# Performance work log

Measured on AMD Instinct MI355X. Metric: run time of the kernel, lower is better.

## Reference

```python
import jax, jax.numpy as jnp
import numpy as np

B, D, U, HU = 2048, 1024, 1024, 256

def _ln(x, eps=1e-3):
    # Keras LayerNormalization(center=False, scale=False), default epsilon=1e-3
    m = jnp.mean(x, axis=-1, keepdims=True)
    v = jnp.var(x, axis=-1, keepdims=True)
    return (x - m) * jax.lax.rsqrt(v + eps)

def setup_inputs() -> dict:
    key = jax.random.key(0)
    ks = jax.random.split(key, 17)
    s = 0.02
    return {
        "inputs": jax.random.normal(ks[0], (B, D), jnp.float32),
        "main_h": 0.1 * jax.random.normal(ks[1], (B, U), jnp.float32),
        "main_c": 0.1 * jax.random.normal(ks[2], (B, U), jnp.float32),
        "hyper_h": 0.1 * jax.random.normal(ks[3], (B, HU), jnp.float32),
        "hyper_c": 0.1 * jax.random.normal(ks[4], (B, HU), jnp.float32),
        "kernel": s * jax.random.normal(ks[5], (D, 4 * U), jnp.float32),
        "recurrent_kernel": s * jax.random.normal(ks[6], (U, 4 * U), jnp.float32),
        "bias": jnp.zeros((4 * U,), jnp.float32),
        "hyper_kernel": s * jax.random.normal(ks[7], (D + U, 4 * HU), jnp.float32),
        "hyper_rec_kernel": s * jax.random.normal(ks[8], (HU, 4 * HU), jnp.float32),
        "hyper_bias": jnp.zeros((4 * HU,), jnp.float32),
        "dx_w": s * jax.random.normal(ks[9], (HU, 4 * U), jnp.float32),
        "dx_b": s * jax.random.normal(ks[10], (4 * U,), jnp.float32),
        "dh_w": s * jax.random.normal(ks[11], (HU, 4 * U), jnp.float32),
        "dh_b": s * jax.random.normal(ks[12], (4 * U,), jnp.float32),
        "db_w": s * jax.random.normal(ks[13], (HU, 4 * U), jnp.float32),
        "db_b": s * jax.random.normal(ks[14], (4 * U,), jnp.float32),
    }

def reference(inputs, main_h, main_c, hyper_h, hyper_c,
              kernel, recurrent_kernel, bias,
              hyper_kernel, hyper_rec_kernel, hyper_bias,
              dx_w, dx_b, dh_w, dh_b, db_w, db_b):
    # --- hyper LSTMCell (Keras gate order i, f, g, o) ---
    hx = jnp.concatenate([inputs, main_h], axis=-1)          # [B, D+U]
    z = hx @ hyper_kernel + hyper_h @ hyper_rec_kernel + hyper_bias  # [B, 4*HU]
    hi, hf, hg, ho = jnp.split(z, 4, axis=-1)
    hyper_c_new = jax.nn.sigmoid(hf) * hyper_c + jax.nn.sigmoid(hi) * jnp.tanh(hg)
    hyper_out = jax.nn.sigmoid(ho) * jnp.tanh(hyper_c_new)  # = hyper_h_new

    # --- hypernet gate scalings ---
    d_x = hyper_out @ dx_w + dx_b                            # [B, 4*U]
    d_h = hyper_out @ dh_w + dh_b
    d_b = hyper_out @ db_w + db_b

    # --- main LSTM gates with hyper modulation + LayerNorm ---
    proj_x = inputs @ kernel + bias                          # [B, 4*U]
    proj_h = main_h @ recurrent_kernel                       # [B, 4*U]
    gates = _ln(d_x * proj_x + d_h * proj_h + d_b)
    i, f, g, o = jnp.split(gates, 4, axis=-1)
    main_c_new = jax.nn.sigmoid(f) * main_c + jax.nn.sigmoid(i) * jnp.tanh(g)
    main_h_new = jax.nn.sigmoid(o) * jnp.tanh(_ln(main_c_new))
    return (main_h_new, main_c_new, hyper_out, hyper_c_new)
```

## Files before the change

kernel.cpp:

```cpp
#include <hip/hip_runtime.h>
#include <cstdint>

typedef unsigned short u16;
typedef _Float16 half8 __attribute__((ext_vector_type(8)));
typedef float floatx4 __attribute__((ext_vector_type(4)));
typedef unsigned short ushort8v __attribute__((ext_vector_type(8)));
typedef float float4v __attribute__((ext_vector_type(4)));

#define BB 2048
#define UU 1024
#define HUx 256
#define O_H  0
#define O_C  (BB*UU)
#define O_HO (2*BB*UU)
#define O_HC (2*BB*UU + BB*HUx)
#define MFMAH __builtin_amdgcn_mfma_f32_16x16x32_f16

#define LBAR() do { \
    asm volatile("s_waitcnt lgkmcnt(0)\n\ts_barrier" ::: "memory"); \
    __builtin_amdgcn_sched_barrier(0); \
} while (0)

__device__ __forceinline__ float bf2f(u16 u) {
    union { uint32_t i; float f; } v; v.i = ((uint32_t)u) << 16; return v.f;
}
__device__ __forceinline__ u16 f2bf(float f) {
    union { float f; uint32_t i; } v; v.f = f;
    uint32_t r = v.i + 0x7fffu + ((v.i >> 16) & 1u);
    return (u16)(r >> 16);
}
__device__ __forceinline__ u16 f2h(float f) {
    _Float16 h = (_Float16)f; u16 u; __builtin_memcpy(&u, &h, 2); return u;
}
__device__ __forceinline__ float sigf(float x) { return 1.f / (1.f + expf(-x)); }
__device__ __forceinline__ float ldmix(const void* p, size_t i, int isbf) {
    return isbf ? bf2f(((const u16*)p)[i]) : ((const float*)p)[i];
}
__device__ __forceinline__ u16 ld2h(const void* p, size_t i, int isbf) {
    return f2h(ldmix(p, i, isbf));
}

__device__ __forceinline__ void ld128(half8 r[2], const u16* src, int row0, int ldK,
                                      int k0, int tid) {
    #pragma unroll
    for (int i = 0; i < 2; i++) {
        int v = tid + 256 * i;
        r[i] = *(const half8*)(src + (size_t)(row0 + (v >> 2)) * ldK + k0 + (v & 3) * 8);
    }
}
__device__ __forceinline__ void ld64(half8& r, const u16* src, int row0, int ldK,
                                     int k0, int tid) {
    r = *(const half8*)(src + (size_t)(row0 + (tid >> 2)) * ldK + k0 + (tid & 3) * 8);
}
__device__ __forceinline__ void wr128(u16* lds, const half8 r[2], int tid) {
    #pragma unroll
    for (int i = 0; i < 2; i++) {
        int v = tid + 256 * i;
        *(half8*)&lds[(v >> 2) * 40 + (v & 3) * 8] = r[i];
    }
}
__device__ __forceinline__ void wr64(u16* lds, half8 r, int tid) {
    *(half8*)&lds[(tid >> 2) * 40 + (tid & 3) * 8] = r;
}
__device__ __forceinline__ void wrS128(u16* lds, const half8 r[2], int tid) {
    #pragma unroll
    for (int i = 0; i < 2; i++) {
        int v = tid + 256 * i;
        int ps = (v & 3) ^ ((v >> 3) & 3);
        *(half8*)&lds[(v >> 2) * 32 + ps * 8] = r[i];
    }
}
__device__ __forceinline__ void wrS64(u16* lds, half8 r, int tid) {
    int ps = (tid & 3) ^ ((tid >> 3) & 3);
    *(half8*)&lds[(tid >> 2) * 32 + ps * 8] = r;
}

__device__ __forceinline__ int detect_local(const u16* raw) {
    int lane = threadIdx.x & 63;
    u16 u = raw[2 * lane];
    int e = (u >> 7) & 0xFF;
    unsigned long long m = __ballot(e >= 100 && e <= 134);
    return (__popcll(m) >= 32) ? 1 : 0;
}

__device__ __forceinline__ void transpose_tile(const void* in, u16* out, int C,
                                               int ostride, int ocol, int r0, int c0,
                                               int isbf, u16 th[32][33]) {
    int tid = threadIdx.x;
    int tx = tid & 31, ty = tid >> 5;
    #pragma unroll
    for (int i = 0; i < 32; i += 8)
        th[ty + i][tx] = ld2h(in, (size_t)(r0 + ty + i) * C + c0 + tx, isbf);
    __syncthreads();
    #pragma unroll
    for (int i = 0; i < 32; i += 8)
        out[(size_t)(c0 + ty + i) * ostride + ocol + r0 + tx] = th[tx][ty + i];
}

__global__ __launch_bounds__(256) void prep_all(
    const void* __restrict__ xs, const void* __restrict__ ms, const void* __restrict__ hs,
    const void* __restrict__ hyper_k, const void* __restrict__ hyper_rk,
    const void* __restrict__ kernel_w, const void* __restrict__ rec_w,
    const void* __restrict__ dx_w, const void* __restrict__ dh_w, const void* __restrict__ db_w,
    u16* __restrict__ xh, u16* __restrict__ mh, u16* __restrict__ hh,
    u16* __restrict__ BTh, u16* __restrict__ kT, u16* __restrict__ rkT,
    u16* __restrict__ dxT, u16* __restrict__ dhT, u16* __restrict__ dbT,
    int* __restrict__ flag) {
    __shared__ u16 th[32][33];
    int bid = blockIdx.x, tid = threadIdx.x;
    int isbf = detect_local((const u16*)xs);
    if (bid == 0 && tid == 0) *flag = isbf;

    if (bid < 2304) {
        int i = bid * 256 + tid;
        const void* src; u16* dst; int t;
        if (i < 262144)      { src = xs; dst = xh; t = i; }
        else if (i < 524288) { src = ms; dst = mh; t = i - 262144; }
        else                 { src = hs; dst = hh; t = i - 524288; }
        half8 o;
        if (isbf) {
            ushort8v v = *(const ushort8v*)((const u16*)src + (size_t)t * 8);
            #pragma unroll
            for (int j = 0; j < 8; j++) o[j] = (_Float16)bf2f(v[j]);
        } else {
            float4v a = *(const float4v*)((const float*)src + (size_t)t * 8);
            float4v b = *(const float4v*)((const float*)src + (size_t)t * 8 + 4);
            #pragma unroll
            for (int j = 0; j < 4; j++) { o[j] = (_Float16)a[j]; o[j + 4] = (_Float16)b[j]; }
        }
        *(half8*)(dst + (size_t)t * 8) = o;
    } else if (bid < 4352) {
        int u = bid - 2304;
        transpose_tile(hyper_k, BTh, 1024, 2304, 0, (u >> 5) * 32, (u & 31) * 32, isbf, th);
    } else if (bid < 4608) {
        int u = bid - 4352;
        transpose_tile(hyper_rk, BTh, 1024, 2304, 2048, (u >> 5) * 32, (u & 31) * 32, isbf, th);
    } else if (bid < 12800) {
        int u = bid - 4608;
        int z = u >> 12;
        int r = u & 4095;
        const void* in = z ? rec_w : kernel_w;
        u16* out = z ? rkT : kT;
        transpose_tile(in, out, 4096, 1024, 0, (r >> 7) * 32, (r & 127) * 32, isbf, th);
    } else {
        int u = bid - 12800;
        int z = u >> 10;
        int r = u & 1023;
        const void* in = (z == 0) ? dx_w : (z == 1) ? dh_w : db_w;
        u16* out = (z == 0) ? dxT : (z == 1) ? dhT : dbT;
        transpose_tile(in, out, 4096, 256, 0, (r >> 7) * 32, (r & 127) * 32, isbf, th);
    }
}

__device__ __forceinline__ void gh_load(half8 pA[2], half8& pB,
                                        const u16* xh, const u16* mh, const u16* hh,
                                        const u16* BT, int bm, int bn, int s, int tid) {
    const u16* Ap; int ldA, kA;
    if (s < 32)      { Ap = xh; ldA = 1024; kA = s * 32; }
    else if (s < 64) { Ap = mh; ldA = 1024; kA = (s - 32) * 32; }
    else             { Ap = hh; ldA = 256;  kA = (s - 64) * 32; }
    ld128(pA, Ap, bm, ldA, kA, tid);
    ld64(pB, BT, bn, 2304, s * 32, tid);
}

__global__ __launch_bounds__(256) void gemm_hyper(const u16* __restrict__ xh,
                                                  const u16* __restrict__ mh,
                                                  const u16* __restrict__ hh,
                                                  const u16* __restrict__ BT,
                                                  float* __restrict__ z) {
    __shared__ __align__(16) u16 sA[128 * 40];
    __shared__ __align__(16) u16 sB[64 * 40];
    int tid = threadIdx.x, lane = tid & 63, wave = tid >> 6;
    int wm = (wave & 1) * 64, wn = (wave >> 1) * 32;
    int bm = blockIdx.y * 128, bn = blockIdx.x * 64;
    int s0 = blockIdx.z * 36, s1 = s0 + 36;
    floatx4 acc[4][2] = {};
    int mr = lane & 15, kq = (lane >> 4) * 8;

    half8 pA[2]; half8 pB;
    gh_load(pA, pB, xh, mh, hh, BT, bm, bn, s0, tid);
    wr128(sA, pA, tid); wr64(sB, pB, tid);
    gh_load(pA, pB, xh, mh, hh, BT, bm, bn, s0 + 1, tid);
    LBAR();

    #pragma unroll 1
    for (int s = s0; s < s1; s++) {
        half8 a[4], b[2];
        #pragma unroll
        for (int t = 0; t < 4; t++) a[t] = *(const half8*)&sA[(wm + t * 16 + mr) * 40 + kq];
        #pragma unroll
        for (int t = 0; t < 2; t++) b[t] = *(const half8*)&sB[(wn + t * 16 + mr) * 40 + kq];
        #pragma unroll
        for (int tm = 0; tm < 4; tm++)
            #pragma unroll
            for (int tn = 0; tn < 2; tn++)
                acc[tm][tn] = MFMAH(a[tm], b[tn], acc[tm][tn], 0, 0, 0);
        LBAR();
        if (s < s1 - 1) {
            wr128(sA, pA, tid); wr64(sB, pB, tid);
            if (s < s1 - 2)
                gh_load(pA, pB, xh, mh, hh, BT, bm, bn, s + 2, tid);
            LBAR();
        }
    }

    float* zp = z + (size_t)blockIdx.z * 2048 * 1024;
    #pragma unroll
    for (int tm = 0; tm < 4; tm++)
        #pragma unroll
        for (int tn = 0; tn < 2; tn++) {
            int col = bn + wn + tn * 16 + (lane & 15);
            #pragma unroll
            for (int rr = 0; rr < 4; rr++) {
                int row = bm + wm + tm * 16 + (lane >> 4) * 4 + rr;
                zp[(size_t)row * 1024 + col] = acc[tm][tn][rr];
            }
        }
}

__global__ void hyper_cell(const float* __restrict__ z, const void* __restrict__ hyper_c,
                           const void* __restrict__ hyper_bias, void* __restrict__ out,
                           u16* __restrict__ ho16, const int* __restrict__ flag) {
    int isbf = *flag;
    int t = blockIdx.x * 256 + threadIdx.x;
    int k = t & 255;
    const float* zr  = z + (size_t)(t >> 8) * 1024;
    const float* zr2 = zr + (size_t)2048 * 1024;
    float hi = zr[k]       + zr2[k]       + ldmix(hyper_bias, k, isbf);
    float hf = zr[k + 256] + zr2[k + 256] + ldmix(hyper_bias, k + 256, isbf);
    float hg = zr[k + 512] + zr2[k + 512] + ldmix(hyper_bias, k + 512, isbf);
    float ho = zr[k + 768] + zr2[k + 768] + ldmix(hyper_bias, k + 768, isbf);
    float c  = ldmix(hyper_c, t, isbf);
    float cn = sigf(hf) * c + sigf(hi) * tanhf(hg);
    float hout = sigf(ho) * tanhf(cn);
    ho16[t] = f2h(hout);
    if (isbf) {
        ((u16*)out)[O_HO + t] = f2bf(hout);
        ((u16*)out)[O_HC + t] = f2bf(cn);
    } else {
        ((float*)out)[O_HO + t] = hout;
        ((float*)out)[O_HC + t] = cn;
    }
}

__global__ __launch_bounds__(256, 2) void mega_fused(
    const u16* __restrict__ xh, const u16* __restrict__ mh, const u16* __restrict__ ho16,
    const u16* __restrict__ kT, const u16* __restrict__ rkT,
    const u16* __restrict__ dxT, const u16* __restrict__ dhT, const u16* __restrict__ dbT,
    const void* __restrict__ bias, const void* __restrict__ dx_b,
    const void* __restrict__ dh_b, const void* __restrict__ db_b,
    u16* __restrict__ gp, const int* __restrict__ flag) {
    __shared__ __align__(16) u16 S[2][12288];
    int isbf = *flag;
    int tid = threadIdx.x, lane = tid & 63, wave = tid >> 6;
    int wm = (wave & 1) * 64, wn = (wave >> 1) * 32;
    int bm = blockIdx.y * 128, bn = blockIdx.x * 64;
    floatx4 apx[4][2] = {}, aph[4][2] = {}, adx[4][2] = {}, adh[4][2] = {}, adb[4][2] = {};
    int mr = lane & 15;
    int kqs = (((lane >> 4) ^ ((mr >> 1) & 3))) * 8;

    half8 nA1[2], nA2[2], nB1, nB2, nB3;

    ld128(nA1, xh,  bm, 1024, 0, tid);
    ld128(nA2, mh,  bm, 1024, 0, tid);
    ld64(nB1, kT,  bn, 1024, 0, tid);
    ld64(nB2, rkT, bn, 1024, 0, tid);
    wrS128(S[0], nA1, tid); wrS128(S[0] + 4096, nA2, tid);
    wrS64(S[0] + 8192, nB1, tid); wrS64(S[0] + 10240, nB2, tid);
    ld128(nA1, xh,  bm, 1024, 32, tid);
    ld128(nA2, mh,  bm, 1024, 32, tid);
    ld64(nB1, kT,  bn, 1024, 32, tid);
    ld64(nB2, rkT, bn, 1024, 32, tid);
    LBAR();

    #pragma unroll 1
    for (int k0 = 0; k0 < 1024; k0 += 32) {
        int p = (k0 >> 5) & 1;
        const u16* C = S[p];
        u16* N = S[p ^ 1];
        half8 ax[4], am[4], bk[2], br[2];
        #pragma unroll
        for (int t = 0; t < 4; t++) {
            int ra = (wm + t * 16 + mr) * 32 + kqs;
            ax[t] = *(const half8*)&C[ra];
            am[t] = *(const half8*)&C[4096 + ra];
        }
        #pragma unroll
        for (int t = 0; t < 2; t++) {
            int rb = (wn + t * 16 + mr) * 32 + kqs;
            bk[t] = *(const half8*)&C[8192 + rb];
            br[t] = *(const half8*)&C[10240 + rb];
        }
        if (k0 < 992) {
            wrS128(N, nA1, tid); wrS128(N + 4096, nA2, tid);
            wrS64(N + 8192, nB1, tid); wrS64(N + 10240, nB2, tid);
        } else {
            wrS128(N, nA1, tid);
            wrS64(N + 8192, nB1, tid); wrS64(N + 10240, nB2, tid); wrS64(N + 4096, nB3, tid);
        }
        if (k0 < 960) {
            ld128(nA1, xh,  bm, 1024, k0 + 64, tid);
            ld128(nA2, mh,  bm, 1024, k0 + 64, tid);
            ld64(nB1, kT,  bn, 1024, k0 + 64, tid);
            ld64(nB2, rkT, bn, 1024, k0 + 64, tid);
        } else if (k0 == 960) {
            ld128(nA1, ho16, bm, 256, 0, tid);
            ld64(nB1, dxT, bn, 256, 0, tid);
            ld64(nB2, dhT, bn, 256, 0, tid);
            ld64(nB3, dbT, bn, 256, 0, tid);
        } else {
            ld128(nA1, ho16, bm, 256, 32, tid);
            ld64(nB1, dxT, bn, 256, 32, tid);
            ld64(nB2, dhT, bn, 256, 32, tid);
            ld64(nB3, dbT, bn, 256, 32, tid);
        }
        #pragma unroll
        for (int tm = 0; tm < 4; tm++)
            #pragma unroll
            for (int tn = 0; tn < 2; tn++) {
                apx[tm][tn] = MFMAH(ax[tm], bk[tn], apx[tm][tn], 0, 0, 0);
                aph[tm][tn] = MFMAH(am[tm], br[tn], aph[tm][tn], 0, 0, 0);
            }
        LBAR();
    }

    #pragma unroll 1
    for (int k0 = 0; k0 < 256; k0 += 32) {
        int p = (k0 >> 5) & 1;
        const u16* C = S[p];
        u16* N = S[p ^ 1];
        half8 a[4], bx[2], bh[2], bb[2];
        #pragma unroll
        for (int t = 0; t < 4; t++) {
            int ra = (wm + t * 16 + mr) * 32 + kqs;
            a[t] = *(const half8*)&C[ra];
        }
        #pragma unroll
        for (int t = 0; t < 2; t++) {
            int rb = (wn + t * 16 + mr) * 32 + kqs;
            bx[t] = *(const half8*)&C[8192 + rb];
            bh[t] = *(const half8*)&C[10240 + rb];
            bb[t] = *(const half8*)&C[4096 + rb];
        }
        if (k0 < 224) {
            wrS128(N, nA1, tid);
            wrS64(N + 8192, nB1, tid); wrS64(N + 10240, nB2, tid); wrS64(N + 4096, nB3, tid);
        }
        if (k0 < 192) {
            ld128(nA1, ho16, bm, 256, k0 + 64, tid);
            ld64(nB1, dxT, bn, 256, k0 + 64, tid);
            ld64(nB2, dhT, bn, 256, k0 + 64, tid);
            ld64(nB3, dbT, bn, 256, k0 + 64, tid);
        }
        #pragma unroll
        for (int tm = 0; tm < 4; tm++)
            #pragma unroll
            for (int tn = 0; tn < 2; tn++) {
                adx[tm][tn] = MFMAH(a[tm], bx[tn], adx[tm][tn], 0, 0, 0);
                adh[tm][tn] = MFMAH(a[tm], bh[tn], adh[tm][tn], 0, 0, 0);
                adb[tm][tn] = MFMAH(a[tm], bb[tn], adb[tm][tn], 0, 0, 0);
            }
        LBAR();
    }

    #pragma unroll
    for (int tn = 0; tn < 2; tn++) {
        int col = bn + wn + tn * 16 + (lane & 15);
        float bv  = ldmix(bias, col, isbf);
        float dxb = ldmix(dx_b, col, isbf);
        float dhb = ldmix(dh_b, col, isbf);
        float dbb = ldmix(db_b, col, isbf);
        #pragma unroll
        for (int tm = 0; tm < 4; tm++) {
            #pragma unroll
            for (int rr = 0; rr < 4; rr++) {
                int row = bm + wm + tm * 16 + (lane >> 4) * 4 + rr;
                float px = apx[tm][tn][rr] + bv;
                float ph = aph[tm][tn][rr];
                float dx = adx[tm][tn][rr] + dxb;
                float dh = adh[tm][tn][rr] + dhb;
                float db = adb[tm][tn][rr] + dbb;
                gp[(size_t)row * 4096 + col] = f2h(dx * px + dh * ph + db);
            }
        }
    }
}

__device__ __forceinline__ void block_reduce2(float& a, float& b, float* red) {
    #pragma unroll
    for (int o = 32; o > 0; o >>= 1) {
        a += __shfl_down(a, o, 64);
        b += __shfl_down(b, o, 64);
    }
    int lane = threadIdx.x & 63, w = threadIdx.x >> 6;
    if (lane == 0) { red[w] = a; red[4 + w] = b; }
    __syncthreads();
    a = red[0] + red[1] + red[2] + red[3];
    b = red[4] + red[5] + red[6] + red[7];
    __syncthreads();
}

__global__ __launch_bounds__(256) void ln_main(const u16* __restrict__ gp,
                                               const void* __restrict__ main_c,
                                               void* __restrict__ out,
                                               const int* __restrict__ flag) {
    __shared__ float sPre[4096];
    __shared__ float sC[1024];
    __shared__ float red[8];
    int isbf = *flag;
    int b = blockIdx.x, tid = threadIdx.x;
    const u16* g = gp + (size_t)b * 4096;
    float s = 0.f, q = 0.f;
    for (int j0 = tid * 8; j0 < 4096; j0 += 2048) {
        half8 v = *(const half8*)(g + j0);
        #pragma unroll
        for (int e = 0; e < 8; e++) {
            float f = (float)v[e];
            sPre[j0 + e] = f; s += f; q += f * f;
        }
    }
    block_reduce2(s, q, red);
    float mean = s * (1.f / 4096.f);
    float var = q * (1.f / 4096.f) - mean * mean;
    float rs = rsqrtf(var + 1e-3f);
    float s2 = 0.f, q2 = 0.f;
    for (int u = tid; u < 1024; u += 256) {
        float gi = (sPre[u] - mean) * rs;
        float gf = (sPre[u + 1024] - mean) * rs;
        float gg = (sPre[u + 2048] - mean) * rs;
        float c = ldmix(main_c, (size_t)b * 1024 + u, isbf);
        float cn = sigf(gf) * c + sigf(gi) * tanhf(gg);
        sC[u] = cn;
        if (isbf) ((u16*)out)[O_C + (size_t)b * 1024 + u] = f2bf(cn);
        else      ((float*)out)[O_C + (size_t)b * 1024 + u] = cn;
        s2 += cn; q2 += cn * cn;
    }
    block_reduce2(s2, q2, red);
    float m2 = s2 * (1.f / 1024.f);
    float v2 = q2 * (1.f / 1024.f) - m2 * m2;
    float rs2 = rsqrtf(v2 + 1e-3f);
    for (int u = tid; u < 1024; u += 256) {
        float go = (sPre[u + 3072] - mean) * rs;
        float hn = sigf(go) * tanhf((sC[u] - m2) * rs2);
        if (isbf) ((u16*)out)[O_H + (size_t)b * 1024 + u] = f2bf(hn);
        else      ((float*)out)[O_H + (size_t)b * 1024 + u] = hn;
    }
}

extern "C" void kernel_launch(void* const* d_in, const int* in_sizes, int n_in,
                              void* d_out, int out_size, void* d_ws, size_t ws_size,
                              hipStream_t stream) {
    (void)in_sizes; (void)n_in; (void)out_size; (void)ws_size;
    const void* inputs   = d_in[0];
    const void* main_h   = d_in[1];
    const void* main_c   = d_in[2];
    const void* hyper_h  = d_in[3];
    const void* hyper_c  = d_in[4];
    const void* kernel_w = d_in[5];
    const void* rec_w    = d_in[6];
    const void* bias     = d_in[7];
    const void* hyper_k  = d_in[8];
    const void* hyper_rk = d_in[9];
    const void* hyper_b  = d_in[10];
    const void* dx_w = d_in[11];
    const void* dx_b = d_in[12];
    const void* dh_w = d_in[13];
    const void* dh_b = d_in[14];
    const void* db_w = d_in[15];
    const void* db_b = d_in[16];
    char* ws = (char*)d_ws;
    const size_t MB = 1024 * 1024;

    int* flag = (int*)ws;
    size_t off = 256;
    u16* xh  = (u16*)(ws + off); off += 4 * MB;
    u16* mh  = (u16*)(ws + off); off += 4 * MB;
    u16* hh  = (u16*)(ws + off); off += 1 * MB;
    u16* ho  = (u16*)(ws + off); off += 1 * MB;
    u16* kT  = (u16*)(ws + off); off += 8 * MB;
    u16* rkT = (u16*)(ws + off); off += 8 * MB;
    u16* dxT = (u16*)(ws + off); off += 2 * MB;
    u16* dhT = (u16*)(ws + off); off += 2 * MB;
    u16* dbT = (u16*)(ws + off); off += 2 * MB;
    u16* BTh = (u16*)(ws + off); off += (size_t)1024 * 2304 * 2;
    float* zbuf = (float*)(ws + off); off += 16 * MB;
    u16* gp    = (u16*)(ws + off); off += 16 * MB;

    prep_all<<<15872, 256, 0, stream>>>(inputs, main_h, hyper_h, hyper_k, hyper_rk,
                                        kernel_w, rec_w, dx_w, dh_w, db_w,
                                        xh, mh, hh, BTh, kT, rkT, dxT, dhT, dbT, flag);
    gemm_hyper<<<dim3(16, 16, 2), 256, 0, stream>>>(xh, mh, hh, BTh, zbuf);
    hyper_cell<<<2048, 256, 0, stream>>>(zbuf, hyper_c, hyper_b, d_out, ho, flag);
    mega_fused<<<dim3(64, 16), 256, 0, stream>>>(xh, mh, ho, kT, rkT, dxT, dhT, dbT,
                                                 bias, dx_b, dh_b, db_b, gp, flag);
    ln_main<<<2048, 256, 0, stream>>>(gp, main_c, d_out, flag);
}
```

Baseline: 269.6 us.

## Overlap main weight transposes with hyper GEMM and vectorize transpose tiles

Moves the transposes of the main, recurrent and hypernet weights out of the prep kernel and into extra blocks of the hyper GEMM launch. Those blocks run alongside the GEMM tiles instead of before them. The transpose tile is rewritten to load and store four elements per thread with a padded shared buffer, so each thread issues fewer, wider memory operations. The GEMM now shares its grid with many memory-bound blocks, so tile scheduling and LDS reuse (sA is used as the transpose scratch) could affect GEMM throughput.

Measured after the change: 259.4 us. 3.8% less time.

```diff
diff --git a/kernel.cpp b/kernel.cpp
--- a/kernel.cpp
+++ b/kernel.cpp
@@ -5,6 +5,7 @@
 typedef _Float16 half8 __attribute__((ext_vector_type(8)));
 typedef float floatx4 __attribute__((ext_vector_type(4)));
 typedef unsigned short ushort8v __attribute__((ext_vector_type(8)));
+typedef unsigned short ushort4v __attribute__((ext_vector_type(4)));
 typedef float float4v __attribute__((ext_vector_type(4)));
 
 #define BB 2048
@@ -83,30 +84,35 @@
     return (__popcll(m) >= 32) ? 1 : 0;
 }
 
-__device__ __forceinline__ void transpose_tile(const void* in, u16* out, int C,
-                                               int ostride, int ocol, int r0, int c0,
-                                               int isbf, u16 th[32][33]) {
+__device__ __forceinline__ void transpose_tile_v(const void* in, u16* out, int C,
+                                                 int ostride, int ocol, int r0, int c0,
+                                                 int isbf, u16* th ) {
     int tid = threadIdx.x;
-    int tx = tid & 31, ty = tid >> 5;
-    #pragma unroll
-    for (int i = 0; i < 32; i += 8)
-        th[ty + i][tx] = ld2h(in, (size_t)(r0 + ty + i) * C + c0 + tx, isbf);
+    int ty = tid >> 3, tx4 = (tid & 7) * 4;
+    ushort4v v;
+    if (isbf) {
+        ushort4v q = *(const ushort4v*)((const u16*)in + (size_t)(r0 + ty) * C + c0 + tx4);
+        #pragma unroll
+        for (int j = 0; j < 4; j++) v[j] = f2h(bf2f(q[j]));
+    } else {
+        float4v q = *(const float4v*)((const float*)in + (size_t)(r0 + ty) * C + c0 + tx4);
+        #pragma unroll
+        for (int j = 0; j < 4; j++) v[j] = f2h(q[j]);
+    }
+    *(ushort4v*)&th[ty * 36 + tx4] = v;
     __syncthreads();
-    #pragma unroll
-    for (int i = 0; i < 32; i += 8)
-        out[(size_t)(c0 + ty + i) * ostride + ocol + r0 + tx] = th[tx][ty + i];
-}
-
-__global__ __launch_bounds__(256) void prep_all(
+    ushort4v w;
+    #pragma unroll
+    for (int j = 0; j < 4; j++) w[j] = th[(tx4 + j) * 36 + ty];
+    *(ushort4v*)(out + (size_t)(c0 + ty) * ostride + ocol + r0 + tx4) = w;
+}
+
+__global__ __launch_bounds__(256) void prep_in(
     const void* __restrict__ xs, const void* __restrict__ ms, const void* __restrict__ hs,
     const void* __restrict__ hyper_k, const void* __restrict__ hyper_rk,
-    const void* __restrict__ kernel_w, const void* __restrict__ rec_w,
-    const void* __restrict__ dx_w, const void* __restrict__ dh_w, const void* __restrict__ db_w,
     u16* __restrict__ xh, u16* __restrict__ mh, u16* __restrict__ hh,
-    u16* __restrict__ BTh, u16* __restrict__ kT, u16* __restrict__ rkT,
-    u16* __restrict__ dxT, u16* __restrict__ dhT, u16* __restrict__ dbT,
-    int* __restrict__ flag) {
-    __shared__ u16 th[32][33];
+    u16* __restrict__ BTh, int* __restrict__ flag) {
+    __shared__ __align__(16) u16 th[32 * 36];
     int bid = blockIdx.x, tid = threadIdx.x;
     int isbf = detect_local((const u16*)xs);
     if (bid == 0 && tid == 0) *flag = isbf;
@@ -131,24 +137,10 @@
         *(half8*)(dst + (size_t)t * 8) = o;
     } else if (bid < 4352) {
         int u = bid - 2304;
-        transpose_tile(hyper_k, BTh, 1024, 2304, 0, (u >> 5) * 32, (u & 31) * 32, isbf, th);
-    } else if (bid < 4608) {
+        transpose_tile_v(hyper_k, BTh, 1024, 2304, 0, (u >> 5) * 32, (u & 31) * 32, isbf, th);
+    } else {
         int u = bid - 4352;
-        transpose_tile(hyper_rk, BTh, 1024, 2304, 2048, (u >> 5) * 32, (u & 31) * 32, isbf, th);
-    } else if (bid < 12800) {
-        int u = bid - 4608;
-        int z = u >> 12;
-        int r = u & 4095;
-        const void* in = z ? rec_w : kernel_w;
-        u16* out = z ? rkT : kT;
-        transpose_tile(in, out, 4096, 1024, 0, (r >> 7) * 32, (r & 127) * 32, isbf, th);
-    } else {
-        int u = bid - 12800;
-        int z = u >> 10;
-        int r = u & 1023;
-        const void* in = (z == 0) ? dx_w : (z == 1) ? dh_w : db_w;
-        u16* out = (z == 0) ? dxT : (z == 1) ? dhT : dbT;
-        transpose_tile(in, out, 4096, 256, 0, (r >> 7) * 32, (r & 127) * 32, isbf, th);
+        transpose_tile_v(hyper_rk, BTh, 1024, 2304, 2048, (u >> 5) * 32, (u & 31) * 32, isbf, th);
     }
 }
 
@@ -163,17 +155,44 @@
     ld64(pB, BT, bn, 2304, s * 32, tid);
 }
 
-__global__ __launch_bounds__(256) void gemm_hyper(const u16* __restrict__ xh,
-                                                  const u16* __restrict__ mh,
-                                                  const u16* __restrict__ hh,
-                                                  const u16* __restrict__ BT,
-                                                  float* __restrict__ z) {
+__global__ __launch_bounds__(256) void gemm_hyper_wt(
+    const u16* __restrict__ xh, const u16* __restrict__ mh, const u16* __restrict__ hh,
+    const u16* __restrict__ BT, float* __restrict__ z,
+    const void* __restrict__ xs,
+    const void* __restrict__ kernel_w, const void* __restrict__ rec_w,
+    const void* __restrict__ dx_w, const void* __restrict__ dh_w,
+    const void* __restrict__ db_w,
+    u16* __restrict__ kT, u16* __restrict__ rkT,
+    u16* __restrict__ dxT, u16* __restrict__ dhT, u16* __restrict__ dbT) {
     __shared__ __align__(16) u16 sA[128 * 40];
     __shared__ __align__(16) u16 sB[64 * 40];
-    int tid = threadIdx.x, lane = tid & 63, wave = tid >> 6;
+    int bid = blockIdx.x, tid = threadIdx.x;
+
+    if (bid >= 512) {
+        int isbf = detect_local((const u16*)xs);
+        int u = bid - 512;
+        const void* in; u16* out; int ostride, r0, c0;
+        if (u < 8192) {
+            in  = (u < 4096) ? kernel_w : rec_w;
+            out = (u < 4096) ? kT : rkT;
+            int r = u & 4095;
+            ostride = 1024; r0 = (r >> 7) * 32; c0 = (r & 127) * 32;
+        } else {
+            int v = u - 8192;
+            int zi = v >> 10, r = v & 1023;
+            in  = (zi == 0) ? dx_w : (zi == 1) ? dh_w : db_w;
+            out = (zi == 0) ? dxT : (zi == 1) ? dhT : dbT;
+            ostride = 256; r0 = (r >> 7) * 32; c0 = (r & 127) * 32;
+        }
+        transpose_tile_v(in, out, 4096, ostride, 0, r0, c0, isbf, sA);
+        return;
+    }
+
+    int bxv = bid & 15, byv = (bid >> 4) & 15, bzv = bid >> 8;
+    int lane = tid & 63, wave = tid >> 6;
     int wm = (wave & 1) * 64, wn = (wave >> 1) * 32;
-    int bm = blockIdx.y * 128, bn = blockIdx.x * 64;
-    int s0 = blockIdx.z * 36, s1 = s0 + 36;
+    int bm = byv * 128, bn = bxv * 64;
+    int s0 = bzv * 36, s1 = s0 + 36;
     floatx4 acc[4][2] = {};
     int mr = lane & 15, kq = (lane >> 4) * 8;
 
@@ -204,7 +223,7 @@
         }
     }
 
-    float* zp = z + (size_t)blockIdx.z * 2048 * 1024;
+    float* zp = z + (size_t)bzv * 2048 * 1024;
     #pragma unroll
     for (int tm = 0; tm < 4; tm++)
         #pragma unroll
@@ -486,10 +505,11 @@
     float* zbuf = (float*)(ws + off); off += 16 * MB;
     u16* gp    = (u16*)(ws + off); off += 16 * MB;
 
-    prep_all<<<15872, 256, 0, stream>>>(inputs, main_h, hyper_h, hyper_k, hyper_rk,
-                                        kernel_w, rec_w, dx_w, dh_w, db_w,
-                                        xh, mh, hh, BTh, kT, rkT, dxT, dhT, dbT, flag);
-    gemm_hyper<<<dim3(16, 16, 2), 256, 0, stream>>>(xh, mh, hh, BTh, zbuf);
+    prep_in<<<4608, 256, 0, stream>>>(inputs, main_h, hyper_h, hyper_k, hyper_rk,
+                                      xh, mh, hh, BTh, flag);
+    gemm_hyper_wt<<<12288, 256, 0, stream>>>(xh, mh, hh, BTh, zbuf, inputs,
+                                             kernel_w, rec_w, dx_w, dh_w, db_w,
+                                             kT, rkT, dxT, dhT, dbT);
     hyper_cell<<<2048, 256, 0, stream>>>(zbuf, hyper_c, hyper_b, d_out, ho, flag);
     mega_fused<<<dim3(64, 16), 256, 0, stream>>>(xh, mh, ho, kT, rkT, dxT, dhT, dbT,
                                                  bias, dx_b, dh_b, db_b, gp, flag);
```
